# Kernel optimization log

Measured on AMD Instinct MI355X. Metric: run time of the kernel, lower is better.

Reference implementation:

```python
import jax, jax.numpy as jnp
import numpy as np

N_NODES = 100000
N_EDGES = 1000000
NUM_FEATURES = 64
HIDDEN = 64
NUM_GRAPHS = 128


def setup_inputs() -> dict:
    key = jax.random.key(0)
    ks = jax.random.split(key, 12)
    x = jax.random.normal(ks[0], (N_NODES, NUM_FEATURES), dtype=jnp.float32)
    edge_index = jax.random.randint(ks[1], (2, N_EDGES), 0, N_NODES, dtype=jnp.int64)
    edge_weight = jax.random.uniform(ks[2], (N_EDGES,), dtype=jnp.float32)
    batch = jnp.sort(jax.random.randint(ks[3], (N_NODES,), 0, NUM_GRAPHS, dtype=jnp.int64))
    s1 = 1.0 / np.sqrt(NUM_FEATURES)
    s2 = 1.0 / np.sqrt(HIDDEN)
    # GraphConv layer 1: lin_rel (with bias) applied to aggregated msgs, lin_root (no bias)
    w1_rel = jax.random.uniform(ks[4], (HIDDEN, NUM_FEATURES), jnp.float32, -s1, s1)
    b1_rel = jax.random.uniform(ks[5], (HIDDEN,), jnp.float32, -s1, s1)
    w1_root = jax.random.uniform(ks[6], (HIDDEN, NUM_FEATURES), jnp.float32, -s1, s1)
    # GraphConv layer 2
    w2_rel = jax.random.uniform(ks[7], (HIDDEN, HIDDEN), jnp.float32, -s2, s2)
    b2_rel = jax.random.uniform(ks[8], (HIDDEN,), jnp.float32, -s2, s2)
    w2_root = jax.random.uniform(ks[9], (HIDDEN, HIDDEN), jnp.float32, -s2, s2)
    # final Linear(hidden, 1)
    w_lin = jax.random.uniform(ks[10], (1, HIDDEN), jnp.float32, -s2, s2)
    b_lin = jax.random.uniform(ks[11], (1,), jnp.float32, -s2, s2)
    return {
        "x": x, "edge_index": edge_index, "edge_weight": edge_weight, "batch": batch,
        "w1_rel": w1_rel, "b1_rel": b1_rel, "w1_root": w1_root,
        "w2_rel": w2_rel, "b2_rel": b2_rel, "w2_root": w2_root,
        "w_lin": w_lin, "b_lin": b_lin,
    }


def graph_conv(x, edge_index, edge_weight, w_rel, b_rel, w_root):
    # messages: x[src] * e, scatter-add into dst  (gather-scale-scatter)
    src, dst = edge_index[0], edge_index[1]
    msgs = x[src] * edge_weight[:, None]                      # [E, F]
    aggr = jax.ops.segment_sum(msgs, dst, num_segments=x.shape[0])  # [N, F]
    return aggr @ w_rel.T + b_rel + x @ w_root.T


def reference(x, edge_index, edge_weight, batch,
              w1_rel, b1_rel, w1_root, w2_rel, b2_rel, w2_root, w_lin, b_lin):
    h = graph_conv(x, edge_index, edge_weight, w1_rel, b1_rel, w1_root)
    h = jax.nn.relu(h)
    h = graph_conv(h, edge_index, edge_weight, w2_rel, b2_rel, w2_root)
    # global_mean_pool over graph ids
    sums = jax.ops.segment_sum(h, batch, num_segments=NUM_GRAPHS)          # [G, H]
    counts = jax.ops.segment_sum(jnp.ones((h.shape[0],), h.dtype), batch,
                                 num_segments=NUM_GRAPHS)                  # [G]
    pooled = sums / jnp.maximum(counts, 1.0)[:, None]
    # dropout(p=0.5) in eval mode is identity
    return pooled @ w_lin.T + b_lin                                        # [G, 1]
```

## Files before the change

### kernel.cpp

```cpp
#include <hip/hip_runtime.h>
#include <hip/hip_bf16.h>


#define N_NODES 100000
#define N_EDGES 1000000
#define NGRAPHS 128
#define BN 512
#define NBUCK ((N_NODES + BN - 1) / BN)
#define FILL_T 16
#define FILL_TILE (256 * FILL_T)
#define FILL_NB ((N_EDGES + FILL_TILE - 1) / FILL_TILE)
#define NTILES (N_NODES / 16)
#define AST 72
#define CVT_NB 3126
#define HIST_NB 256
#define N16 (N_NODES * 64 / 16)

typedef __attribute__((ext_vector_type(8))) short bf16x8;
typedef __attribute__((ext_vector_type(8))) unsigned short u16x8;
typedef __attribute__((ext_vector_type(4))) float f32x4;
typedef __attribute__((ext_vector_type(2))) float f32x2;

__device__ __forceinline__ unsigned short f2bf(float f) {
    unsigned u = __float_as_uint(f);
    unsigned r = (u + 0x7FFFu + ((u >> 16) & 1u)) >> 16;
    return (unsigned short)r;
}
__device__ __forceinline__ float bf2f(unsigned short h) {
    return __uint_as_float(((unsigned)h) << 16);
}
__device__ __forceinline__ void fma4(int w, float wt, float* a) {
    f32x2 lo = __builtin_amdgcn_cvt_pk_f32_fp8(w, false);
    f32x2 hi = __builtin_amdgcn_cvt_pk_f32_fp8(w, true);
    a[0] += wt * lo[0];
    a[1] += wt * lo[1];
    a[2] += wt * hi[0];
    a[3] += wt * hi[1];
}
__device__ __forceinline__ int pack4(float f0, float f1, float f2, float f3) {
    int w = __builtin_amdgcn_cvt_pk_fp8_f32(f0, f1, 0, false);
    w = __builtin_amdgcn_cvt_pk_fp8_f32(f2, f3, w, true);
    return w;
}

__global__ __launch_bounds__(256) void prep_cvt_hist_kernel(
    const float* __restrict__ x, unsigned short* __restrict__ xh, int n8,
    const float* __restrict__ w1rel, const float* __restrict__ w1root,
    const float* __restrict__ w2rel, const float* __restrict__ w2root,
    const float* __restrict__ wlin, const float* __restrict__ b2rel,
    const float* __restrict__ blin, unsigned short* __restrict__ whirel,
    unsigned short* __restrict__ wlorel, unsigned short* __restrict__ whiroot,
    unsigned short* __restrict__ wloroot, float* __restrict__ u,
    float* __restrict__ v, float* __restrict__ C,
    const int* __restrict__ ei, int* __restrict__ bcount, int E) {
    int tid = threadIdx.x;
    if (blockIdx.x >= CVT_NB) {
        __shared__ int lh[NBUCK];
        for (int i = tid; i < NBUCK; i += 256) lh[i] = 0;
        __syncthreads();
        int bid2 = blockIdx.x - CVT_NB;
        for (int e = bid2 * 256 + tid; e < E; e += HIST_NB * 256)
            atomicAdd(&lh[ei[E + e] >> 9], 1);
        __syncthreads();
        for (int i = tid; i < NBUCK; i += 256) {
            int c = lh[i];
            if (c) atomicAdd(&bcount[i], c);
        }
        return;
    }
    int i = blockIdx.x * 256 + tid;
    if (i < n8) {
        const float4* xp = (const float4*)x + (size_t)i * 2;
        float4 a = xp[0], b = xp[1];
        u16x8 o;
        o[0] = f2bf(a.x); o[1] = f2bf(a.y); o[2] = f2bf(a.z); o[3] = f2bf(a.w);
        o[4] = f2bf(b.x); o[5] = f2bf(b.y); o[6] = f2bf(b.z); o[7] = f2bf(b.w);
        *((u16x8*)xh + i) = o;
        return;
    }
    for (int k = tid; k < 4096; k += 256) {
        float a = w1rel[k];
        unsigned short hi = f2bf(a);
        whirel[k] = hi;
        wlorel[k] = f2bf(a - bf2f(hi));
        float b = w1root[k];
        unsigned short hb = f2bf(b);
        whiroot[k] = hb;
        wloroot[k] = f2bf(b - bf2f(hb));
    }
    if (tid < 64) {
        float uu = 0.f, vv = 0.f;
        for (int h = 0; h < 64; ++h) {
            float wl = wlin[h];
            uu += wl * w2rel[h * 64 + tid];
            vv += wl * w2root[h * 64 + tid];
        }
        u[tid] = uu;
        v[tid] = vv;
    }
    if (tid == 0) {
        float c = blin[0];
        for (int h = 0; h < 64; ++h) c += wlin[h] * b2rel[h];
        *C = c;
    }
}

__global__ void bucket_scan(const int* __restrict__ bcount,
                            int* __restrict__ boff, int* __restrict__ cursor) {
    __shared__ int s[256];
    int t = threadIdx.x;
    int v = (t < NBUCK) ? bcount[t] : 0;
    s[t] = v;
    __syncthreads();
    for (int off = 1; off < 256; off <<= 1) {
        int x = (t >= off) ? s[t - off] : 0;
        __syncthreads();
        s[t] += x;
        __syncthreads();
    }
    if (t < NBUCK) {
        boff[t] = s[t] - v;
        cursor[t] = s[t] - v;
    }
    if (t == 255) boff[NBUCK] = s[255];
}

__global__ __launch_bounds__(256) void bucket_fill(
    const int* __restrict__ ei, const float* __restrict__ ew,
    int* __restrict__ cursor, int2* __restrict__ ebuf, int E) {
    __shared__ int lh[NBUCK];
    __shared__ int gbase[NBUCK];
    int tid = threadIdx.x;
    for (int i = tid; i < NBUCK; i += 256) lh[i] = 0;
    __syncthreads();
    int base = blockIdx.x * FILL_TILE;
    int2 rec[FILL_T];
    int meta[FILL_T];
#pragma unroll
    for (int i = 0; i < FILL_T; ++i) {
        int e = base + i * 256 + tid;
        meta[i] = -1;
        if (e < E) {
            int src = ei[e];
            int dst = ei[E + e];
            int b = dst >> 9;
            int r = atomicAdd(&lh[b], 1);
            rec[i].x = src | ((dst & (BN - 1)) << 17);
            rec[i].y = __float_as_int(ew[e]);
            meta[i] = (b << 13) | r;
        }
    }
    __syncthreads();
    for (int i = tid; i < NBUCK; i += 256) {
        int c = lh[i];
        gbase[i] = c ? atomicAdd(&cursor[i], c) : 0;
    }
    __syncthreads();
#pragma unroll
    for (int i = 0; i < FILL_T; ++i) {
        if (meta[i] >= 0) {
            int b = meta[i] >> 13;
            int r = meta[i] & 8191;
            ebuf[gbase[b] + r] = rec[i];
        }
    }
}

__global__ __launch_bounds__(512) void csr_build(
    const int* __restrict__ boff, const int2* __restrict__ ebuf,
    const int* __restrict__ batch, int* __restrict__ row_ptr,
    int2* __restrict__ csr, int N) {
    __shared__ int s[BN];
    int b = blockIdx.x;
    int t = threadIdx.x;
    int beg = boff[b], end = boff[b + 1];
    s[t] = 0;
    __syncthreads();
    for (int j = beg + t; j < end; j += 512)
        atomicAdd(&s[(ebuf[j].x >> 17) & (BN - 1)], 1);
    __syncthreads();
    int v = s[t];
    for (int off = 1; off < BN; off <<= 1) {
        int x = (t >= off) ? s[t - off] : 0;
        __syncthreads();
        s[t] += x;
        __syncthreads();
    }
    int excl = s[t] - v;
    int gidx = b * BN + t;
    if (gidx <= N) row_ptr[gidx] = beg + excl;
    __syncthreads();
    s[t] = excl;
    __syncthreads();
    for (int j = beg + t; j < end; j += 512) {
        int2 rec = ebuf[j];
        int dlo = (rec.x >> 17) & (BN - 1);
        int g = batch[b * BN + dlo];
        int r = atomicAdd(&s[dlo], 1);
        int2 o;
        o.x = (rec.x & 0x1FFFF) | (g << 17);
        o.y = rec.y;
        csr[beg + r] = o;
    }
}

__global__ __launch_bounds__(256) void cvt8_kernel(
    const unsigned short* __restrict__ xh, int* __restrict__ xf8) {
    int i = blockIdx.x * 256 + threadIdx.x;
    if (i >= N16) return;
    const u16x8* src = (const u16x8*)xh + (size_t)i * 2;
    u16x8 h0 = src[0], h1 = src[1];
    int4 o;
    o.x = pack4(bf2f(h0[0]), bf2f(h0[1]), bf2f(h0[2]), bf2f(h0[3]));
    o.y = pack4(bf2f(h0[4]), bf2f(h0[5]), bf2f(h0[6]), bf2f(h0[7]));
    o.z = pack4(bf2f(h1[0]), bf2f(h1[1]), bf2f(h1[2]), bf2f(h1[3]));
    o.w = pack4(bf2f(h1[4]), bf2f(h1[5]), bf2f(h1[6]), bf2f(h1[7]));
    ((int4*)xf8)[i] = o;
}

__global__ __launch_bounds__(256) void gather_dense_kernel(
    const unsigned char* __restrict__ xf8, const unsigned short* __restrict__ xh,
    const int* __restrict__ row_ptr, const int2* __restrict__ csr,
    const unsigned short* __restrict__ whirel,
    const unsigned short* __restrict__ wlorel,
    const unsigned short* __restrict__ whiroot,
    const unsigned short* __restrict__ wloroot,
    const float* __restrict__ b1rel, const float* __restrict__ u,
    const float* __restrict__ v, float* __restrict__ p, float* __restrict__ q,
    int ntiles) {
    __shared__ unsigned short arow[4][16 * AST];
    int lane = threadIdx.x & 63;
    int wv = threadIdx.x >> 6;
    int wave = (blockIdx.x << 2) + wv;
    if (wave >= ntiles) return;
    unsigned short* my = &arow[wv][0];
    int nb = wave * 16;

    {
        int g4 = lane >> 2;
        int c4 = lane & 3;
        int node = nb + g4;
        int beg = row_ptr[node], end = row_ptr[node + 1];
        float a0[16], a1[16];
#pragma unroll
        for (int t = 0; t < 16; ++t) { a0[t] = 0.f; a1[t] = 0.f; }
        const unsigned char* xb = xf8 + (size_t)c4 * 16;
        int j = beg;
        for (; j + 2 <= end; j += 2) {
            int2 e0 = csr[j];
            int2 e1 = csr[j + 1];
            int4 r0 = *(const int4*)(xb + (size_t)(e0.x & 0x1FFFF) * 64);
            int4 r1 = *(const int4*)(xb + (size_t)(e1.x & 0x1FFFF) * 64);
            float w0 = __int_as_float(e0.y);
            float w1 = __int_as_float(e1.y);
            fma4(r0.x, w0, a0 + 0);
            fma4(r0.y, w0, a0 + 4);
            fma4(r0.z, w0, a0 + 8);
            fma4(r0.w, w0, a0 + 12);
            fma4(r1.x, w1, a1 + 0);
            fma4(r1.y, w1, a1 + 4);
            fma4(r1.z, w1, a1 + 8);
            fma4(r1.w, w1, a1 + 12);
        }
        if (j < end) {
            int2 e0 = csr[j];
            int4 r0 = *(const int4*)(xb + (size_t)(e0.x & 0x1FFFF) * 64);
            float w0 = __int_as_float(e0.y);
            fma4(r0.x, w0, a0 + 0);
            fma4(r0.y, w0, a0 + 4);
            fma4(r0.z, w0, a0 + 8);
            fma4(r0.w, w0, a0 + 12);
        }
        u16x8 o0, o1;
#pragma unroll
        for (int t = 0; t < 8; ++t) {
            o0[t] = f2bf(a0[t] + a1[t]);
            o1[t] = f2bf(a0[8 + t] + a1[8 + t]);
        }
        *(u16x8*)(my + g4 * AST + c4 * 16) = o0;
        *(u16x8*)(my + g4 * AST + c4 * 16 + 8) = o1;
    }

    int lo4 = lane & 15;
    int quad = lane >> 4;
    f32x4 acc4[4];
#pragma unroll
    for (int t = 0; t < 4; ++t) acc4[t] = (f32x4){0.f, 0.f, 0.f, 0.f};
#pragma unroll
    for (int s = 0; s < 2; ++s) {
        bf16x8 Aa = *(const bf16x8*)(my + lo4 * AST + s * 32 + quad * 8);
        bf16x8 Ax = *(const bf16x8*)(xh + (size_t)(nb + lo4) * 64 + s * 32 +
                                     quad * 8);
#pragma unroll
        for (int t = 0; t < 4; ++t) {
            int off = (t * 16 + lo4) * 64 + s * 32 + quad * 8;
            bf16x8 bhr = *(const bf16x8*)(whirel + off);
            bf16x8 blr = *(const bf16x8*)(wlorel + off);
            bf16x8 bhx = *(const bf16x8*)(whiroot + off);
            bf16x8 blx = *(const bf16x8*)(wloroot + off);
            acc4[t] = __builtin_amdgcn_mfma_f32_16x16x32_bf16(Aa, bhr, acc4[t],
                                                              0, 0, 0);
            acc4[t] = __builtin_amdgcn_mfma_f32_16x16x32_bf16(Aa, blr, acc4[t],
                                                              0, 0, 0);
            acc4[t] = __builtin_amdgcn_mfma_f32_16x16x32_bf16(Ax, bhx, acc4[t],
                                                              0, 0, 0);
            acc4[t] = __builtin_amdgcn_mfma_f32_16x16x32_bf16(Ax, blx, acc4[t],
                                                              0, 0, 0);
        }
    }

    float pc[4] = {0.f, 0.f, 0.f, 0.f};
    float qc[4] = {0.f, 0.f, 0.f, 0.f};
#pragma unroll
    for (int t = 0; t < 4; ++t) {
        float bb = b1rel[t * 16 + lo4];
        float uu = u[t * 16 + lo4];
        float vv = v[t * 16 + lo4];
#pragma unroll
        for (int r = 0; r < 4; ++r) {
            float h1 = fmaxf(acc4[t][r] + bb, 0.f);
            pc[r] += uu * h1;
            qc[r] += vv * h1;
        }
    }
#pragma unroll
    for (int off = 1; off < 16; off <<= 1) {
#pragma unroll
        for (int r = 0; r < 4; ++r) {
            pc[r] += __shfl_xor(pc[r], off);
            qc[r] += __shfl_xor(qc[r], off);
        }
    }
    if (lo4 == 0) {
        f32x4 po = {pc[0], pc[1], pc[2], pc[3]};
        f32x4 qo = {qc[0], qc[1], qc[2], qc[3]};
        *(f32x4*)(p + nb + quad * 4) = po;
        *(f32x4*)(q + nb + quad * 4) = qo;
    }
}

#define PT_EPT 4
#define PT_EPW (64 * PT_EPT)
#define PT_NB ((N_EDGES + 4 * PT_EPW - 1) / (4 * PT_EPW))
#define PS_NB 98
__global__ __launch_bounds__(256) void pool_both(
    const int2* __restrict__ csr, const float* __restrict__ p,
    const float* __restrict__ q, const int* __restrict__ batch,
    float* __restrict__ gp, float* __restrict__ gq, float* __restrict__ gc,
    int* __restrict__ done, const float* __restrict__ C,
    float* __restrict__ out, int E, int N) {
    __shared__ float lbuf[2 * NGRAPHS];
    __shared__ int amLast;
    int tid = threadIdx.x;
    lbuf[tid] = 0.f;
    __syncthreads();
    if (blockIdx.x < PT_NB) {
        int lane = tid & 63;
        int wid = (blockIdx.x * 256 + tid) >> 6;
        int base = wid * PT_EPW;
        float acc = 0.f;
        int curg = -1;
#pragma unroll
        for (int i = 0; i < PT_EPT; ++i) {
            int j = base + i * 64 + lane;
            if (j < E) {
                int2 e = csr[j];
                int g = ((unsigned)e.x) >> 17;
                float val = __int_as_float(e.y) * p[e.x & 0x1FFFF];
                if (g != curg) {
                    if (curg >= 0) atomicAdd(&lbuf[curg], acc);
                    curg = g;
                    acc = 0.f;
                }
                acc += val;
            }
        }
        if (curg >= 0) atomicAdd(&lbuf[curg], acc);
        __syncthreads();
        if (tid < NGRAPHS) {
            float t = lbuf[tid];
            if (t != 0.f) atomicAdd(&gp[tid], t);
        }
    } else {
        int bid = blockIdx.x - PT_NB;
        for (int i = bid * 256 + tid; i < N; i += PS_NB * 256) {
            int g = batch[i];
            atomicAdd(&lbuf[g], q[i]);
            atomicAdd(&lbuf[NGRAPHS + g], 1.f);
        }
        __syncthreads();
        if (tid < NGRAPHS) {
            if (lbuf[NGRAPHS + tid] != 0.f) {
                atomicAdd(&gq[tid], lbuf[tid]);
                atomicAdd(&gc[tid], lbuf[NGRAPHS + tid]);
            }
        }
    }
    __syncthreads();
    if (tid == 0) {
        __threadfence();
        amLast = (atomicAdd(done, 1) == PT_NB + PS_NB - 1);
    }
    __syncthreads();
    if (amLast) {
        __threadfence();
        if (tid < NGRAPHS) {
            float pv = atomicAdd(&gp[tid], 0.f);
            float qv = atomicAdd(&gq[tid], 0.f);
            float cv = atomicAdd(&gc[tid], 0.f);
            out[tid] = (pv + qv) / fmaxf(cv, 1.f) + C[0];
        }
    }
}

extern "C" void kernel_launch(void* const* d_in, const int* in_sizes, int n_in,
                              void* d_out, int out_size, void* d_ws,
                              size_t ws_size, hipStream_t stream) {
    const float* x      = (const float*)d_in[0];
    const int*   ei     = (const int*)d_in[1];
    const float* ew     = (const float*)d_in[2];
    const int*   batch  = (const int*)d_in[3];
    const float* w1rel  = (const float*)d_in[4];
    const float* b1rel  = (const float*)d_in[5];
    const float* w1root = (const float*)d_in[6];
    const float* w2rel  = (const float*)d_in[7];
    const float* b2rel  = (const float*)d_in[8];
    const float* w2root = (const float*)d_in[9];
    const float* wlin   = (const float*)d_in[10];
    const float* blin   = (const float*)d_in[11];
    float* out = (float*)d_out;

    char* wsb = (char*)d_ws;
    int2* csr  = (int2*)wsb;
    int2* ebuf = (int2*)(wsb + (size_t)N_EDGES * 8);
    int*  xf8  = (int*)ebuf;
    char* tail = wsb + (size_t)N_EDGES * 16;
    unsigned short* whirel  = (unsigned short*)tail;
    unsigned short* wlorel  = whirel + 4096;
    unsigned short* whiroot = wlorel + 4096;
    unsigned short* wloroot = whiroot + 4096;
    float* p  = (float*)(wloroot + 4096);
    float* q  = p + N_NODES;
    float* u  = q + N_NODES;
    float* v  = u + 64;
    float* C  = v + 64;
    int*   bcount = (int*)(C + 1);
    float* gp = (float*)(bcount + NBUCK);
    float* gq = gp + NGRAPHS;
    float* gc = gq + NGRAPHS;
    int*   done   = (int*)(gc + NGRAPHS);
    int*   boff   = done + 1;
    int*   cursor = boff + (NBUCK + 1);
    int*   row_ptr = cursor + NBUCK;
    unsigned short* xh = (unsigned short*)(row_ptr + N_NODES + 2);

    hipMemsetAsync(bcount, 0, (NBUCK + 3 * NGRAPHS + 1) * sizeof(int), stream);

    int n8 = N_NODES * 64 / 8;
    prep_cvt_hist_kernel<<<CVT_NB + HIST_NB, 256, 0, stream>>>(
        x, xh, n8, w1rel, w1root, w2rel, w2root, wlin, b2rel, blin, whirel,
        wlorel, whiroot, wloroot, u, v, C, ei, bcount, N_EDGES);

    bucket_scan<<<1, 256, 0, stream>>>(bcount, boff, cursor);
    bucket_fill<<<FILL_NB, 256, 0, stream>>>(ei, ew, cursor, ebuf, N_EDGES);
    csr_build<<<NBUCK, 512, 0, stream>>>(boff, ebuf, batch, row_ptr, csr,
                                         N_NODES);
    cvt8_kernel<<<(N16 + 255) / 256, 256, 0, stream>>>(xh, xf8);

    gather_dense_kernel<<<(NTILES + 3) / 4, 256, 0, stream>>>(
        (const unsigned char*)xf8, xh, row_ptr, csr, whirel, wlorel, whiroot,
        wloroot, b1rel, u, v, p, q, NTILES);

    pool_both<<<PT_NB + PS_NB, 256, 0, stream>>>(csr, p, q, batch, gp, gq, gc,
                                                 done, C, out, N_EDGES,
                                                 N_NODES);
}
```

Baseline: 218.0 us.

## Fuse conversion, scans and pooling stages to cut kernel launches and passes

The fp8 conversion now happens in the prep kernel straight from fp32, and graph counts are computed there too, so the separate cvt8 kernel is gone. The bucket scan is recomputed redundantly inside bucket_fill and csr_build, which removes the single-block scan kernel. The q pooling is folded into the gather kernel through atomics, and the gather loop is unrolled to four edges with clamped indices. This saves several launches and a pass over the node array, at the cost of repeated scans, more global atomics and wasted loads on padded edges.

```diff
diff --git a/kernel.cpp b/kernel.cpp
--- a/kernel.cpp
+++ b/kernel.cpp
@@ -12,9 +12,13 @@
 #define FILL_NB ((N_EDGES + FILL_TILE - 1) / FILL_TILE)
 #define NTILES (N_NODES / 16)
 #define AST 72
-#define CVT_NB 3126
+
+#define PREP_CVT_NB 3125
+#define HIST0 (PREP_CVT_NB + 1)
 #define HIST_NB 256
-#define N16 (N_NODES * 64 / 16)
+#define CNT0 (HIST0 + HIST_NB)
+#define CNT_NB 64
+#define PREP_TOTAL (CNT0 + CNT_NB)
 
 typedef __attribute__((ext_vector_type(8))) short bf16x8;
 typedef __attribute__((ext_vector_type(8))) unsigned short u16x8;
@@ -43,8 +47,9 @@
     return w;
 }
 
-__global__ __launch_bounds__(256) void prep_cvt_hist_kernel(
-    const float* __restrict__ x, unsigned short* __restrict__ xh, int n8,
+__global__ __launch_bounds__(256) void prep_all_kernel(
+    const float* __restrict__ x, unsigned short* __restrict__ xh,
+    int* __restrict__ xf8,
     const float* __restrict__ w1rel, const float* __restrict__ w1root,
     const float* __restrict__ w2rel, const float* __restrict__ w2root,
     const float* __restrict__ wlin, const float* __restrict__ b2rel,
@@ -52,86 +57,100 @@
     unsigned short* __restrict__ wlorel, unsigned short* __restrict__ whiroot,
     unsigned short* __restrict__ wloroot, float* __restrict__ u,
     float* __restrict__ v, float* __restrict__ C,
-    const int* __restrict__ ei, int* __restrict__ bcount, int E) {
+    const int* __restrict__ ei, int* __restrict__ bcount,
+    const int* __restrict__ batch, float* __restrict__ gc, int E) {
     int tid = threadIdx.x;
-    if (blockIdx.x >= CVT_NB) {
-        __shared__ int lh[NBUCK];
-        for (int i = tid; i < NBUCK; i += 256) lh[i] = 0;
-        __syncthreads();
-        int bid2 = blockIdx.x - CVT_NB;
-        for (int e = bid2 * 256 + tid; e < E; e += HIST_NB * 256)
-            atomicAdd(&lh[ei[E + e] >> 9], 1);
-        __syncthreads();
-        for (int i = tid; i < NBUCK; i += 256) {
-            int c = lh[i];
-            if (c) atomicAdd(&bcount[i], c);
-        }
-        return;
-    }
-    int i = blockIdx.x * 256 + tid;
-    if (i < n8) {
+    if (blockIdx.x < PREP_CVT_NB) {
+        int i = blockIdx.x * 256 + tid;
         const float4* xp = (const float4*)x + (size_t)i * 2;
         float4 a = xp[0], b = xp[1];
         u16x8 o;
         o[0] = f2bf(a.x); o[1] = f2bf(a.y); o[2] = f2bf(a.z); o[3] = f2bf(a.w);
         o[4] = f2bf(b.x); o[5] = f2bf(b.y); o[6] = f2bf(b.z); o[7] = f2bf(b.w);
         *((u16x8*)xh + i) = o;
+        int2 o8;
+        o8.x = pack4(a.x, a.y, a.z, a.w);
+        o8.y = pack4(b.x, b.y, b.z, b.w);
+        *((int2*)xf8 + i) = o8;
         return;
     }
-    for (int k = tid; k < 4096; k += 256) {
-        float a = w1rel[k];
-        unsigned short hi = f2bf(a);
-        whirel[k] = hi;
-        wlorel[k] = f2bf(a - bf2f(hi));
-        float b = w1root[k];
-        unsigned short hb = f2bf(b);
-        whiroot[k] = hb;
-        wloroot[k] = f2bf(b - bf2f(hb));
-    }
-    if (tid < 64) {
-        float uu = 0.f, vv = 0.f;
-        for (int h = 0; h < 64; ++h) {
-            float wl = wlin[h];
-            uu += wl * w2rel[h * 64 + tid];
-            vv += wl * w2root[h * 64 + tid];
-        }
-        u[tid] = uu;
-        v[tid] = vv;
-    }
-    if (tid == 0) {
-        float c = blin[0];
-        for (int h = 0; h < 64; ++h) c += wlin[h] * b2rel[h];
-        *C = c;
-    }
-}
-
-__global__ void bucket_scan(const int* __restrict__ bcount,
-                            int* __restrict__ boff, int* __restrict__ cursor) {
-    __shared__ int s[256];
-    int t = threadIdx.x;
-    int v = (t < NBUCK) ? bcount[t] : 0;
-    s[t] = v;
-    __syncthreads();
-    for (int off = 1; off < 256; off <<= 1) {
-        int x = (t >= off) ? s[t - off] : 0;
-        __syncthreads();
-        s[t] += x;
-        __syncthreads();
-    }
-    if (t < NBUCK) {
-        boff[t] = s[t] - v;
-        cursor[t] = s[t] - v;
-    }
-    if (t == 255) boff[NBUCK] = s[255];
+    if (blockIdx.x == PREP_CVT_NB) {
+        for (int k = tid; k < 4096; k += 256) {
+            float a = w1rel[k];
+            unsigned short hi = f2bf(a);
+            whirel[k] = hi;
+            wlorel[k] = f2bf(a - bf2f(hi));
+            float b = w1root[k];
+            unsigned short hb = f2bf(b);
+            whiroot[k] = hb;
+            wloroot[k] = f2bf(b - bf2f(hb));
+        }
+        if (tid < 64) {
+            float uu = 0.f, vv = 0.f;
+            for (int h = 0; h < 64; ++h) {
+                float wl = wlin[h];
+                uu += wl * w2rel[h * 64 + tid];
+                vv += wl * w2root[h * 64 + tid];
+            }
+            u[tid] = uu;
+            v[tid] = vv;
+        }
+        if (tid == 0) {
+            float c = blin[0];
+            for (int h = 0; h < 64; ++h) c += wlin[h] * b2rel[h];
+            *C = c;
+        }
+        return;
+    }
+    if (blockIdx.x < CNT0) {
+        __shared__ int lh[NBUCK];
+        for (int i = tid; i < NBUCK; i += 256) lh[i] = 0;
+        __syncthreads();
+        int bid2 = blockIdx.x - HIST0;
+        for (int e = bid2 * 256 + tid; e < E; e += HIST_NB * 256)
+            atomicAdd(&lh[ei[E + e] >> 9], 1);
+        __syncthreads();
+        for (int i = tid; i < NBUCK; i += 256) {
+            int c = lh[i];
+            if (c) atomicAdd(&bcount[i], c);
+        }
+        return;
+    }
+    {
+        __shared__ int lgc[NGRAPHS];
+        for (int i = tid; i < NGRAPHS; i += 256) lgc[i] = 0;
+        __syncthreads();
+        int bid2 = blockIdx.x - CNT0;
+        for (int i = bid2 * 256 + tid; i < N_NODES; i += CNT_NB * 256)
+            atomicAdd(&lgc[batch[i]], 1);
+        __syncthreads();
+        for (int i = tid; i < NGRAPHS; i += 256) {
+            int c = lgc[i];
+            if (c) atomicAdd(&gc[i], (float)c);
+        }
+    }
 }
 
 __global__ __launch_bounds__(256) void bucket_fill(
     const int* __restrict__ ei, const float* __restrict__ ew,
-    int* __restrict__ cursor, int2* __restrict__ ebuf, int E) {
+    const int* __restrict__ bcount, int* __restrict__ cursor,
+    int2* __restrict__ ebuf, int E) {
     __shared__ int lh[NBUCK];
     __shared__ int gbase[NBUCK];
+    __shared__ int sc[256];
+    __shared__ int lbo[NBUCK];
     int tid = threadIdx.x;
     for (int i = tid; i < NBUCK; i += 256) lh[i] = 0;
+    int v = (tid < NBUCK) ? bcount[tid] : 0;
+    sc[tid] = v;
+    __syncthreads();
+    for (int off = 1; off < 256; off <<= 1) {
+        int x = (tid >= off) ? sc[tid - off] : 0;
+        __syncthreads();
+        sc[tid] += x;
+        __syncthreads();
+    }
+    if (tid < NBUCK) lbo[tid] = sc[tid] - v;
     __syncthreads();
     int base = blockIdx.x * FILL_TILE;
     int2 rec[FILL_T];
@@ -153,7 +172,7 @@
     __syncthreads();
     for (int i = tid; i < NBUCK; i += 256) {
         int c = lh[i];
-        gbase[i] = c ? atomicAdd(&cursor[i], c) : 0;
+        gbase[i] = c ? (lbo[i] + atomicAdd(&cursor[i], c)) : 0;
     }
     __syncthreads();
 #pragma unroll
@@ -167,13 +186,24 @@
 }
 
 __global__ __launch_bounds__(512) void csr_build(
-    const int* __restrict__ boff, const int2* __restrict__ ebuf,
+    const int* __restrict__ bcount, const int2* __restrict__ ebuf,
     const int* __restrict__ batch, int* __restrict__ row_ptr,
     int2* __restrict__ csr, int N) {
     __shared__ int s[BN];
     int b = blockIdx.x;
     int t = threadIdx.x;
-    int beg = boff[b], end = boff[b + 1];
+    int vv = (t < NBUCK) ? bcount[t] : 0;
+    if (t < 256) s[t] = vv;
+    __syncthreads();
+    for (int off = 1; off < 256; off <<= 1) {
+        int x = (t >= off && t < 256) ? s[t - off] : 0;
+        __syncthreads();
+        if (t < 256) s[t] += x;
+        __syncthreads();
+    }
+    int beg = (b == 0) ? 0 : s[b - 1];
+    int end = s[b];
+    __syncthreads();
     s[t] = 0;
     __syncthreads();
     for (int j = beg + t; j < end; j += 512)
@@ -204,30 +234,17 @@
     }
 }
 
-__global__ __launch_bounds__(256) void cvt8_kernel(
-    const unsigned short* __restrict__ xh, int* __restrict__ xf8) {
-    int i = blockIdx.x * 256 + threadIdx.x;
-    if (i >= N16) return;
-    const u16x8* src = (const u16x8*)xh + (size_t)i * 2;
-    u16x8 h0 = src[0], h1 = src[1];
-    int4 o;
-    o.x = pack4(bf2f(h0[0]), bf2f(h0[1]), bf2f(h0[2]), bf2f(h0[3]));
-    o.y = pack4(bf2f(h0[4]), bf2f(h0[5]), bf2f(h0[6]), bf2f(h0[7]));
-    o.z = pack4(bf2f(h1[0]), bf2f(h1[1]), bf2f(h1[2]), bf2f(h1[3]));
-    o.w = pack4(bf2f(h1[4]), bf2f(h1[5]), bf2f(h1[6]), bf2f(h1[7]));
-    ((int4*)xf8)[i] = o;
-}
-
 __global__ __launch_bounds__(256) void gather_dense_kernel(
     const unsigned char* __restrict__ xf8, const unsigned short* __restrict__ xh,
     const int* __restrict__ row_ptr, const int2* __restrict__ csr,
+    const int* __restrict__ batch,
     const unsigned short* __restrict__ whirel,
     const unsigned short* __restrict__ wlorel,
     const unsigned short* __restrict__ whiroot,
     const unsigned short* __restrict__ wloroot,
     const float* __restrict__ b1rel, const float* __restrict__ u,
-    const float* __restrict__ v, float* __restrict__ p, float* __restrict__ q,
-    int ntiles) {
+    const float* __restrict__ v, float* __restrict__ p,
+    float* __restrict__ gq, int ntiles) {
     __shared__ unsigned short arow[4][16 * AST];
     int lane = threadIdx.x & 63;
     int wv = threadIdx.x >> 6;
@@ -241,41 +258,48 @@
         int c4 = lane & 3;
         int node = nb + g4;
         int beg = row_ptr[node], end = row_ptr[node + 1];
-        float a0[16], a1[16];
-#pragma unroll
-        for (int t = 0; t < 16; ++t) { a0[t] = 0.f; a1[t] = 0.f; }
+        float a[16];
+#pragma unroll
+        for (int t = 0; t < 16; ++t) a[t] = 0.f;
         const unsigned char* xb = xf8 + (size_t)c4 * 16;
-        int j = beg;
-        for (; j + 2 <= end; j += 2) {
+        for (int j = beg; j < end; j += 4) {
+            int i1 = min(j + 1, end - 1);
+            int i2 = min(j + 2, end - 1);
+            int i3 = min(j + 3, end - 1);
             int2 e0 = csr[j];
-            int2 e1 = csr[j + 1];
+            int2 e1 = csr[i1];
+            int2 e2 = csr[i2];
+            int2 e3 = csr[i3];
             int4 r0 = *(const int4*)(xb + (size_t)(e0.x & 0x1FFFF) * 64);
             int4 r1 = *(const int4*)(xb + (size_t)(e1.x & 0x1FFFF) * 64);
+            int4 r2 = *(const int4*)(xb + (size_t)(e2.x & 0x1FFFF) * 64);
+            int4 r3 = *(const int4*)(xb + (size_t)(e3.x & 0x1FFFF) * 64);
             float w0 = __int_as_float(e0.y);
-            float w1 = __int_as_float(e1.y);
-            fma4(r0.x, w0, a0 + 0);
-            fma4(r0.y, w0, a0 + 4);
-            fma4(r0.z, w0, a0 + 8);
-            fma4(r0.w, w0, a0 + 12);
-            fma4(r1.x, w1, a1 + 0);
-            fma4(r1.y, w1, a1 + 4);
-            fma4(r1.z, w1, a1 + 8);
-            fma4(r1.w, w1, a1 + 12);
-        }
-        if (j < end) {
-            int2 e0 = csr[j];
-            int4 r0 = *(const int4*)(xb + (size_t)(e0.x & 0x1FFFF) * 64);
-            float w0 = __int_as_float(e0.y);
-            fma4(r0.x, w0, a0 + 0);
-            fma4(r0.y, w0, a0 + 4);
-            fma4(r0.z, w0, a0 + 8);
-            fma4(r0.w, w0, a0 + 12);
+            float w1 = (j + 1 < end) ? __int_as_float(e1.y) : 0.f;
+            float w2 = (j + 2 < end) ? __int_as_float(e2.y) : 0.f;
+            float w3 = (j + 3 < end) ? __int_as_float(e3.y) : 0.f;
+            fma4(r0.x, w0, a + 0);
+            fma4(r0.y, w0, a + 4);
+            fma4(r0.z, w0, a + 8);
+            fma4(r0.w, w0, a + 12);
+            fma4(r1.x, w1, a + 0);
+            fma4(r1.y, w1, a + 4);
+            fma4(r1.z, w1, a + 8);
+            fma4(r1.w, w1, a + 12);
+            fma4(r2.x, w2, a + 0);
+            fma4(r2.y, w2, a + 4);
+            fma4(r2.z, w2, a + 8);
+            fma4(r2.w, w2, a + 12);
+            fma4(r3.x, w3, a + 0);
+            fma4(r3.y, w3, a + 4);
+            fma4(r3.z, w3, a + 8);
+            fma4(r3.w, w3, a + 12);
         }
         u16x8 o0, o1;
 #pragma unroll
         for (int t = 0; t < 8; ++t) {
-            o0[t] = f2bf(a0[t] + a1[t]);
-            o1[t] = f2bf(a0[8 + t] + a1[8 + t]);
+            o0[t] = f2bf(a[t]);
+            o1[t] = f2bf(a[8 + t]);
         }
         *(u16x8*)(my + g4 * AST + c4 * 16) = o0;
         *(u16x8*)(my + g4 * AST + c4 * 16 + 8) = o1;
@@ -333,81 +357,66 @@
     }
     if (lo4 == 0) {
         f32x4 po = {pc[0], pc[1], pc[2], pc[3]};
-        f32x4 qo = {qc[0], qc[1], qc[2], qc[3]};
         *(f32x4*)(p + nb + quad * 4) = po;
-        *(f32x4*)(q + nb + quad * 4) = qo;
+#pragma unroll
+        for (int r = 0; r < 4; ++r) {
+            int g = batch[nb + quad * 4 + r];
+            atomicAdd(&gq[g], qc[r]);
+        }
     }
 }
 
 #define PT_EPT 4
 #define PT_EPW (64 * PT_EPT)
 #define PT_NB ((N_EDGES + 4 * PT_EPW - 1) / (4 * PT_EPW))
-#define PS_NB 98
-__global__ __launch_bounds__(256) void pool_both(
+__global__ __launch_bounds__(256) void pool_t(
     const int2* __restrict__ csr, const float* __restrict__ p,
-    const float* __restrict__ q, const int* __restrict__ batch,
-    float* __restrict__ gp, float* __restrict__ gq, float* __restrict__ gc,
-    int* __restrict__ done, const float* __restrict__ C,
-    float* __restrict__ out, int E, int N) {
-    __shared__ float lbuf[2 * NGRAPHS];
+    float* __restrict__ gp, const float* __restrict__ gq,
+    const float* __restrict__ gc, int* __restrict__ done,
+    const float* __restrict__ C, float* __restrict__ out, int E) {
+    __shared__ float lbuf[NGRAPHS];
     __shared__ int amLast;
     int tid = threadIdx.x;
-    lbuf[tid] = 0.f;
-    __syncthreads();
-    if (blockIdx.x < PT_NB) {
-        int lane = tid & 63;
-        int wid = (blockIdx.x * 256 + tid) >> 6;
-        int base = wid * PT_EPW;
-        float acc = 0.f;
-        int curg = -1;
-#pragma unroll
-        for (int i = 0; i < PT_EPT; ++i) {
-            int j = base + i * 64 + lane;
-            if (j < E) {
-                int2 e = csr[j];
-                int g = ((unsigned)e.x) >> 17;
-                float val = __int_as_float(e.y) * p[e.x & 0x1FFFF];
-                if (g != curg) {
-                    if (curg >= 0) atomicAdd(&lbuf[curg], acc);
-                    curg = g;
-                    acc = 0.f;
-                }
-                acc += val;
+    if (tid < NGRAPHS) lbuf[tid] = 0.f;
+    __syncthreads();
+    int lane = tid & 63;
+    int wid = (blockIdx.x * 256 + tid) >> 6;
+    int base = wid * PT_EPW;
+    float acc = 0.f;
+    int curg = -1;
+#pragma unroll
+    for (int i = 0; i < PT_EPT; ++i) {
+        int j = base + i * 64 + lane;
+        if (j < E) {
+            int2 e = csr[j];
+            int g = ((unsigned)e.x) >> 17;
+            float val = __int_as_float(e.y) * p[e.x & 0x1FFFF];
+            if (g != curg) {
+                if (curg >= 0) atomicAdd(&lbuf[curg], acc);
+                curg = g;
+                acc = 0.f;
             }
-        }
-        if (curg >= 0) atomicAdd(&lbuf[curg], acc);
-        __syncthreads();
-        if (tid < NGRAPHS) {
-            float t = lbuf[tid];
-            if (t != 0.f) atomicAdd(&gp[tid], t);
-        }
-    } else {
-        int bid = blockIdx.x - PT_NB;
-        for (int i = bid * 256 + tid; i < N; i += PS_NB * 256) {
-            int g = batch[i];
-            atomicAdd(&lbuf[g], q[i]);
-            atomicAdd(&lbuf[NGRAPHS + g], 1.f);
-        }
-        __syncthreads();
-        if (tid < NGRAPHS) {
-            if (lbuf[NGRAPHS + tid] != 0.f) {
-                atomicAdd(&gq[tid], lbuf[tid]);
-                atomicAdd(&gc[tid], lbuf[NGRAPHS + tid]);
-            }
-        }
+            acc += val;
+        }
+    }
+    if (curg >= 0) atomicAdd(&lbuf[curg], acc);
+    __syncthreads();
+    if (tid < NGRAPHS) {
+        float t = lbuf[tid];
+        if (t != 0.f) atomicAdd(&gp[tid], t);
     }
     __syncthreads();
     if (tid == 0) {
         __threadfence();
-        amLast = (atomicAdd(done, 1) == PT_NB + PS_NB - 1);
+        amLast = (atomicAdd(done, 1) == PT_NB - 1);
     }
     __syncthreads();
     if (amLast) {
         __threadfence();
         if (tid < NGRAPHS) {
             float pv = atomicAdd(&gp[tid], 0.f);
-            float qv = atomicAdd(&gq[tid], 0.f);
-            float cv = atomicAdd(&gc[tid], 0.f);
+            float qv = atomicAdd((float*)&gq[tid], 0.f);
+            float cv = atomicAdd((float*)&gc[tid], 0.f);
             out[tid] = (pv + qv) / fmaxf(cv, 1.f) + C[0];
         }
     }
@@ -433,15 +442,13 @@
     char* wsb = (char*)d_ws;
     int2* csr  = (int2*)wsb;
     int2* ebuf = (int2*)(wsb + (size_t)N_EDGES * 8);
-    int*  xf8  = (int*)ebuf;
     char* tail = wsb + (size_t)N_EDGES * 16;
     unsigned short* whirel  = (unsigned short*)tail;
     unsigned short* wlorel  = whirel + 4096;
     unsigned short* whiroot = wlorel + 4096;
     unsigned short* wloroot = whiroot + 4096;
     float* p  = (float*)(wloroot + 4096);
-    float* q  = p + N_NODES;
-    float* u  = q + N_NODES;
+    float* u  = p + N_NODES;
     float* v  = u + 64;
     float* C  = v + 64;
     int*   bcount = (int*)(C + 1);
@@ -449,29 +456,27 @@
     float* gq = gp + NGRAPHS;
     float* gc = gq + NGRAPHS;
     int*   done   = (int*)(gc + NGRAPHS);
-    int*   boff   = done + 1;
-    int*   cursor = boff + (NBUCK + 1);
+    int*   cursor = done + 1;
     int*   row_ptr = cursor + NBUCK;
     unsigned short* xh = (unsigned short*)(row_ptr + N_NODES + 2);
-
-    hipMemsetAsync(bcount, 0, (NBUCK + 3 * NGRAPHS + 1) * sizeof(int), stream);
-
-    int n8 = N_NODES * 64 / 8;
-    prep_cvt_hist_kernel<<<CVT_NB + HIST_NB, 256, 0, stream>>>(
-        x, xh, n8, w1rel, w1root, w2rel, w2root, wlin, b2rel, blin, whirel,
-        wlorel, whiroot, wloroot, u, v, C, ei, bcount, N_EDGES);
-
-    bucket_scan<<<1, 256, 0, stream>>>(bcount, boff, cursor);
-    bucket_fill<<<FILL_NB, 256, 0, stream>>>(ei, ew, cursor, ebuf, N_EDGES);
-    csr_build<<<NBUCK, 512, 0, stream>>>(boff, ebuf, batch, row_ptr, csr,
+    int*   xf8 = (int*)(xh + (size_t)N_NODES * 64);
+
+    hipMemsetAsync(bcount, 0, (2 * NBUCK + 3 * NGRAPHS + 1) * sizeof(int),
+                   stream);
+
+    prep_all_kernel<<<PREP_TOTAL, 256, 0, stream>>>(
+        x, xh, xf8, w1rel, w1root, w2rel, w2root, wlin, b2rel, blin, whirel,
+        wlorel, whiroot, wloroot, u, v, C, ei, bcount, batch, gc, N_EDGES);
+
+    bucket_fill<<<FILL_NB, 256, 0, stream>>>(ei, ew, bcount, cursor, ebuf,
+                                             N_EDGES);
+    csr_build<<<NBUCK, 512, 0, stream>>>(bcount, ebuf, batch, row_ptr, csr,
                                          N_NODES);
-    cvt8_kernel<<<(N16 + 255) / 256, 256, 0, stream>>>(xh, xf8);
 
     gather_dense_kernel<<<(NTILES + 3) / 4, 256, 0, stream>>>(
-        (const unsigned char*)xf8, xh, row_ptr, csr, whirel, wlorel, whiroot,
-        wloroot, b1rel, u, v, p, q, NTILES);
-
-    pool_both<<<PT_NB + PS_NB, 256, 0, stream>>>(csr, p, q, batch, gp, gq, gc,
-                                                 done, C, out, N_EDGES,
-                                                 N_NODES);
-}
+        (const unsigned char*)xf8, xh, row_ptr, csr, batch, whirel, wlorel,
+        whiroot, wloroot, b1rel, u, v, p, gq, NTILES);
+
+    pool_t<<<PT_NB, 256, 0, stream>>>(csr, p, gp, gq, gc, done, C, out,
+                                      N_EDGES);
+}
```

Result: slower. 576.5 us (+164.5%).
